# Performance work log

Hardware: AMD Instinct MI355X
Metric: run time of the kernel (lower is better)

## Reference

```python
import jax, jax.numpy as jnp
import numpy as np

# Config matching init_kwargs
DILATED = (1, 2, 3)
K = 4            # proto_size
P = 96           # num_prototypes
NUM_CLASSES = 2
E = 1024         # enc_size (bert-large)
EPS = 1e-8       # torch F.cosine_similarity eps
NUM_FILTERS = (32, 32, 32)  # P // len(DILATED) per dilation


def _neg_cosine_dist(batch, p_flat, d):
    """Replicates F.unfold(kernel=(K,1), dilation=d) + view(N,1,H,K*E) + -cosine_similarity.

    batch:  (N, S, E)
    p_flat: (n, K*E) -- protolayer slice flattened exactly as torch .view does
    returns (N, n, H) with H = S - d*(K-1)
    """
    N, S, _ = batch.shape
    H = S - d * (K - 1)
    # torch unfold output is (N, K, H*E) with element [n,k,h*E+e] = batch[n, h+k*d, e];
    # the subsequent .view(N,1,H,K*E) row-major reinterprets (K,H,E) -> (H, K*E).
    x = jnp.stack([batch[:, k * d:k * d + H, :] for k in range(K)], axis=1)  # (N, K, H, E)
    x = x.reshape(N, H, K * E)  # identical flattening to torch view
    dot = jnp.einsum('nhm,pm->nph', x, p_flat)              # (N, n, H)
    xn = jnp.maximum(jnp.linalg.norm(x, axis=-1), EPS)      # (N, H)
    pn = jnp.maximum(jnp.linalg.norm(p_flat, axis=-1), EPS)  # (n,)
    cos = dot / (xn[:, None, :] * pn[None, :, None])
    return -cos


def setup_inputs() -> dict:
    key = jax.random.key(0)
    k1, k2, k3 = jax.random.split(key, 3)
    N, S = 16, 512
    embedding = jax.random.normal(k1, (N, S, E), dtype=jnp.float32)
    mask = jnp.ones((N, S), dtype=jnp.int64)
    # nn.init.uniform_ default range [0, 1)
    protolayer = jax.random.uniform(k2, (P, E, K), dtype=jnp.float32)
    fc_w = jax.random.normal(k3, (NUM_CLASSES, P), dtype=jnp.float32) * 0.1
    return {"embedding": embedding, "mask": mask, "protolayer": protolayer, "fc_w": fc_w}


def reference(embedding, mask, protolayer, fc_w):
    # protolayer (P, E, K) -> (P, K*E) exactly as torch .view(1, P, 1, K*E)
    p_flat = protolayer.reshape(P, K * E)
    dists = []
    j = 0
    for d, n in zip(DILATED, NUM_FILTERS):
        dists.append(_neg_cosine_dist(embedding, p_flat[j:j + n], d))
        j += n
    # min-pool over sliding-window positions, concat over prototype groups
    prototype_distances = jnp.concatenate([jnp.min(x, axis=2) for x in dists], axis=1)  # (N, P)
    class_out = prototype_distances @ fc_w.T  # Linear(bias=False)
    return prototype_distances, class_out
```

## Files before the change

### kernel.cpp

```cpp
#include <hip/hip_runtime.h>
#include <stdint.h>

#define EE 1024
#define SS 512
#define NBATCH 16
#define PP 96
#define NROWS (NBATCH * SS)
#define NJ (PP * 4)
#define EPS 1e-8f

typedef __attribute__((ext_vector_type(8))) short bf16x8;
typedef __attribute__((ext_vector_type(4))) float f32x4;

__device__ __forceinline__ ushort f2bf(float f) {
    uint32_t u = __float_as_uint(f);
    u += 0x7fffu + ((u >> 16) & 1u);
    return (ushort)(u >> 16);
}

__device__ __forceinline__ void gload16(const void* g, void* l) {
    __builtin_amdgcn_global_load_lds(
        (const __attribute__((address_space(1))) uint32_t*)g,
        (__attribute__((address_space(3))) uint32_t*)l, 16, 0, 0);
}

__global__ __launch_bounds__(256) void conv_emb_kernel(const float* __restrict__ emb,
                                                       ushort* __restrict__ ebf,
                                                       float* __restrict__ rn2) {
    int r = blockIdx.x, t = threadIdx.x;
    float4 v = ((const float4*)(emb + (size_t)r * EE))[t];
    ((ushort4*)(ebf + (size_t)r * EE))[t] =
        make_ushort4(f2bf(v.x), f2bf(v.y), f2bf(v.z), f2bf(v.w));
    float s = v.x * v.x + v.y * v.y + v.z * v.z + v.w * v.w;
#pragma unroll
    for (int off = 32; off; off >>= 1) s += __shfl_down(s, off);
    __shared__ float red[4];
    if ((t & 63) == 0) red[t >> 6] = s;
    __syncthreads();
    if (t == 0) rn2[r] = red[0] + red[1] + red[2] + red[3];
}

__global__ __launch_bounds__(256) void conv_proto_kernel(const float* __restrict__ proto,
                                                         ushort* __restrict__ pbf,
                                                         float* __restrict__ pn) {
    int p = blockIdx.x, t = threadIdx.x;
    const float4* src = (const float4*)(proto + (size_t)p * 4096);
    ushort4* dst = (ushort4*)(pbf + (size_t)p * 4096);
    float s = 0.f;
#pragma unroll
    for (int i = 0; i < 4; i++) {
        float4 v = src[t + 256 * i];
        dst[t + 256 * i] = make_ushort4(f2bf(v.x), f2bf(v.y), f2bf(v.z), f2bf(v.w));
        s += v.x * v.x + v.y * v.y + v.z * v.z + v.w * v.w;
    }
#pragma unroll
    for (int off = 32; off; off >>= 1) s += __shfl_down(s, off);
    __shared__ float red[4];
    if ((t & 63) == 0) red[t >> 6] = s;
    __syncthreads();
    if (t == 0) pn[p] = sqrtf(red[0] + red[1] + red[2] + red[3]);
}

#define GBM 128
#define GBN 128
#define GBK 32

__global__ __launch_bounds__(256) void gemm_kernel(const ushort* __restrict__ A,
                                                   const ushort* __restrict__ B,
                                                   float* __restrict__ Rt,
                                                   int nsplit) {
    __shared__ ushort As[GBM * GBK];
    __shared__ ushort Bs[GBN * GBK];
    const int per = (NROWS / GBM) * (NJ / GBN);
    int bid = blockIdx.x;
    int split = bid / per;
    int rem = bid - split * per;
    int bm = rem & 63;
    int bn = rem >> 6;
    int klen = EE / nsplit;
    int kb = split * klen;
    int r0 = bm * GBM, j0 = bn * GBN;
    int tid = threadIdx.x;
    int lane = tid & 63;

    int srow = tid >> 2;
    int schunk = (tid & 3) ^ (srow & 3);
    const ushort* ga = A + (size_t)(r0 + srow) * EE + kb + schunk * 8;
    const ushort* gb = B + (size_t)(j0 + srow) * EE + kb + schunk * 8;
    ushort* lA = As + tid * 8;
    ushort* lB = Bs + tid * 8;

    int w = tid >> 6;
    int wm = (w >> 1) * 64, wn = (w & 1) * 64;
    int kc = lane >> 4;
    int fr = lane & 15;
    int fchunk = kc ^ (fr & 3);

    f32x4 acc[4][4] = {};

    for (int k0 = 0; k0 < klen; k0 += GBK) {
        __syncthreads();
        gload16(ga + k0, lA);
        gload16(ga + 64 * EE + k0, lA + 2048);
        gload16(gb + k0, lB);
        gload16(gb + 64 * EE + k0, lB + 2048);
        __syncthreads();
        bf16x8 af[4], bfr[4];
#pragma unroll
        for (int m = 0; m < 4; m++)
            af[m] = *(const bf16x8*)(As + (wm + m * 16 + fr) * GBK + fchunk * 8);
#pragma unroll
        for (int n = 0; n < 4; n++)
            bfr[n] = *(const bf16x8*)(Bs + (wn + n * 16 + fr) * GBK + fchunk * 8);
#pragma unroll
        for (int m = 0; m < 4; m++)
#pragma unroll
            for (int n = 0; n < 4; n++)
                acc[m][n] = __builtin_amdgcn_mfma_f32_16x16x32_bf16(af[m], bfr[n], acc[m][n], 0, 0, 0);
    }

    float* Rbase = Rt + (size_t)split * NJ * NROWS;
    int rloc = r0 + wm + (lane >> 4) * 4;
    int jloc = j0 + wn + fr;
#pragma unroll
    for (int m = 0; m < 4; m++)
#pragma unroll
        for (int n = 0; n < 4; n++)
            *(f32x4*)(Rbase + (size_t)(jloc + n * 16) * NROWS + rloc + m * 16) = acc[m][n];
}

__global__ __launch_bounds__(256) void combine_kernel(const float* __restrict__ Rt,
                                                      const float* __restrict__ rn2,
                                                      const float* __restrict__ pn,
                                                      float* __restrict__ out, int nsplit) {
    int wave = threadIdx.x >> 6;
    int lane = threadIdx.x & 63;
    int pair = blockIdx.x * 4 + wave;
    int n = pair / PP;
    int p = pair % PP;
    int d = (p >> 5) + 1;
    int H = SS - 3 * d;
    float pnv = fmaxf(pn[p], EPS);
    float best = -3.4e38f;
    for (int h = lane; h < H; h += 64) {
        float dot = 0.f, x2 = 0.f;
#pragma unroll
        for (int j = 0; j < 4; j++) {
            int q = h * 4 + j;
            int k = q / H;
            int s = q - k * H + k * d;
            int r = n * SS + s;
            size_t off = (size_t)(4 * p + j) * NROWS + r;
            float dv = Rt[off];
            if (nsplit == 2) dv += Rt[(size_t)NJ * NROWS + off];
            dot += dv;
            x2 += rn2[r];
        }
        float xn = fmaxf(sqrtf(x2), EPS);
        best = fmaxf(best, dot / (xn * pnv));
    }
#pragma unroll
    for (int off = 32; off; off >>= 1) best = fmaxf(best, __shfl_down(best, off));
    if (lane == 0) out[n * PP + p] = -best;
}

__global__ __launch_bounds__(64) void fc_kernel(const float* __restrict__ pd,
                                                const float* __restrict__ fcw,
                                                float* __restrict__ cls) {
    int t = threadIdx.x;
    if (t >= 32) return;
    int n = t >> 1, c = t & 1;
    float s = 0.f;
    for (int p = 0; p < PP; p++) s += pd[n * PP + p] * fcw[c * PP + p];
    cls[n * 2 + c] = s;
}

extern "C" void kernel_launch(void* const* d_in, const int* in_sizes, int n_in,
                              void* d_out, int out_size, void* d_ws, size_t ws_size,
                              hipStream_t stream) {
    const float* emb = (const float*)d_in[0];
    const float* proto = (const float*)d_in[2];
    const float* fcw = (const float*)d_in[3];
    float* out = (float*)d_out;

    uint8_t* ws = (uint8_t*)d_ws;
    ushort* ebf = (ushort*)ws;
    ushort* pbf = (ushort*)(ws + (size_t)NROWS * EE * 2);
    float* rn2 = (float*)(ws + (size_t)NROWS * EE * 2 + (size_t)NJ * EE * 2);
    float* pn = rn2 + NROWS;
    float* Rt = pn + 128;
    size_t fixed = (size_t)NROWS * EE * 2 + (size_t)NJ * EE * 2 + (size_t)(NROWS + 128) * 4;
    int nsplit = (ws_size >= fixed + 2 * (size_t)NJ * NROWS * 4) ? 2 : 1;

    conv_emb_kernel<<<NROWS, 256, 0, stream>>>(emb, ebf, rn2);
    conv_proto_kernel<<<PP, 256, 0, stream>>>(proto, pbf, pn);
    gemm_kernel<<<192 * nsplit, 256, 0, stream>>>(ebf, pbf, Rt, nsplit);
    combine_kernel<<<NBATCH * PP / 4, 256, 0, stream>>>(Rt, rn2, pn, out, nsplit);
    fc_kernel<<<1, 64, 0, stream>>>(out, fcw, out + NBATCH * PP);
}
```

Baseline: 53.66 us.

## Fuse conversion kernels, retile GEMM without split-K, fold FC into combine

Merges the embedding and prototype bf16 conversion into one launch, with one wave per embedding row. The GEMM is retiled to 64x128 tiles with a 64-wide K step and an 8-chunk swizzle, which replaces the split-K path with 384 blocks over the full K range. The final linear layer is folded into the combine kernel through atomicAdd onto a cls buffer zeroed with a memset. This reduces launch count and the extra split-K partial-sum traffic, but adds a memset launch and float atomics whose summation order is nondeterministic.

```diff
diff --git a/kernel.cpp b/kernel.cpp
--- a/kernel.cpp
+++ b/kernel.cpp
@@ -24,115 +24,129 @@
         (__attribute__((address_space(3))) uint32_t*)l, 16, 0, 0);
 }
 
-__global__ __launch_bounds__(256) void conv_emb_kernel(const float* __restrict__ emb,
-                                                       ushort* __restrict__ ebf,
-                                                       float* __restrict__ rn2) {
-    int r = blockIdx.x, t = threadIdx.x;
-    float4 v = ((const float4*)(emb + (size_t)r * EE))[t];
-    ((ushort4*)(ebf + (size_t)r * EE))[t] =
-        make_ushort4(f2bf(v.x), f2bf(v.y), f2bf(v.z), f2bf(v.w));
-    float s = v.x * v.x + v.y * v.y + v.z * v.z + v.w * v.w;
-#pragma unroll
-    for (int off = 32; off; off >>= 1) s += __shfl_down(s, off);
-    __shared__ float red[4];
-    if ((t & 63) == 0) red[t >> 6] = s;
-    __syncthreads();
-    if (t == 0) rn2[r] = red[0] + red[1] + red[2] + red[3];
-}
-
-__global__ __launch_bounds__(256) void conv_proto_kernel(const float* __restrict__ proto,
-                                                         ushort* __restrict__ pbf,
-                                                         float* __restrict__ pn) {
-    int p = blockIdx.x, t = threadIdx.x;
-    const float4* src = (const float4*)(proto + (size_t)p * 4096);
-    ushort4* dst = (ushort4*)(pbf + (size_t)p * 4096);
-    float s = 0.f;
-#pragma unroll
-    for (int i = 0; i < 4; i++) {
-        float4 v = src[t + 256 * i];
-        dst[t + 256 * i] = make_ushort4(f2bf(v.x), f2bf(v.y), f2bf(v.z), f2bf(v.w));
-        s += v.x * v.x + v.y * v.y + v.z * v.z + v.w * v.w;
-    }
-#pragma unroll
-    for (int off = 32; off; off >>= 1) s += __shfl_down(s, off);
-    __shared__ float red[4];
-    if ((t & 63) == 0) red[t >> 6] = s;
-    __syncthreads();
-    if (t == 0) pn[p] = sqrtf(red[0] + red[1] + red[2] + red[3]);
-}
-
-#define GBM 128
+__global__ __launch_bounds__(256) void conv_kernel(const float* __restrict__ emb,
+                                                   const float* __restrict__ proto,
+                                                   ushort* __restrict__ ebf,
+                                                   ushort* __restrict__ pbf,
+                                                   float* __restrict__ rn2,
+                                                   float* __restrict__ pn) {
+    int b = blockIdx.x, t = threadIdx.x;
+    if (b < NROWS / 4) {
+        int r = b * 4 + (t >> 6);
+        int l = t & 63;
+        const float4* src = (const float4*)(emb + (size_t)r * EE);
+        ushort4* dst = (ushort4*)(ebf + (size_t)r * EE);
+        float s = 0.f;
+#pragma unroll
+        for (int i = 0; i < 4; i++) {
+            float4 v = src[l + 64 * i];
+            dst[l + 64 * i] = make_ushort4(f2bf(v.x), f2bf(v.y), f2bf(v.z), f2bf(v.w));
+            s += v.x * v.x + v.y * v.y + v.z * v.z + v.w * v.w;
+        }
+#pragma unroll
+        for (int off = 32; off; off >>= 1) s += __shfl_down(s, off);
+        if (l == 0) rn2[r] = s;
+    } else {
+        int p = b - NROWS / 4;
+        const float4* src = (const float4*)(proto + (size_t)p * 4096);
+        ushort4* dst = (ushort4*)(pbf + (size_t)p * 4096);
+        float s = 0.f;
+#pragma unroll
+        for (int i = 0; i < 4; i++) {
+            float4 v = src[t + 256 * i];
+            dst[t + 256 * i] = make_ushort4(f2bf(v.x), f2bf(v.y), f2bf(v.z), f2bf(v.w));
+            s += v.x * v.x + v.y * v.y + v.z * v.z + v.w * v.w;
+        }
+#pragma unroll
+        for (int off = 32; off; off >>= 1) s += __shfl_down(s, off);
+        __shared__ float red[4];
+        if ((t & 63) == 0) red[t >> 6] = s;
+        __syncthreads();
+        if (t == 0) pn[p] = sqrtf(red[0] + red[1] + red[2] + red[3]);
+    }
+}
+
+#define GBM 64
 #define GBN 128
-#define GBK 32
+#define GBK 64
 
 __global__ __launch_bounds__(256) void gemm_kernel(const ushort* __restrict__ A,
                                                    const ushort* __restrict__ B,
-                                                   float* __restrict__ Rt,
-                                                   int nsplit) {
+                                                   float* __restrict__ Rt) {
     __shared__ ushort As[GBM * GBK];
     __shared__ ushort Bs[GBN * GBK];
-    const int per = (NROWS / GBM) * (NJ / GBN);
-    int bid = blockIdx.x;
-    int split = bid / per;
-    int rem = bid - split * per;
-    int bm = rem & 63;
-    int bn = rem >> 6;
-    int klen = EE / nsplit;
-    int kb = split * klen;
+    int bn = blockIdx.x >> 7;
+    int bm = blockIdx.x & 127;
     int r0 = bm * GBM, j0 = bn * GBN;
     int tid = threadIdx.x;
     int lane = tid & 63;
 
-    int srow = tid >> 2;
-    int schunk = (tid & 3) ^ (srow & 3);
-    const ushort* ga = A + (size_t)(r0 + srow) * EE + kb + schunk * 8;
-    const ushort* gb = B + (size_t)(j0 + srow) * EE + kb + schunk * 8;
+    int srow = tid >> 3;
+    int gc = (tid & 7) ^ (srow & 7);
+    const ushort* ga = A + (size_t)(r0 + srow) * EE + gc * 8;
+    const ushort* gb = B + (size_t)(j0 + srow) * EE + gc * 8;
     ushort* lA = As + tid * 8;
     ushort* lB = Bs + tid * 8;
 
     int w = tid >> 6;
-    int wm = (w >> 1) * 64, wn = (w & 1) * 64;
+    int wm = (w >> 1) * 32, wn = (w & 1) * 64;
     int kc = lane >> 4;
     int fr = lane & 15;
-    int fchunk = kc ^ (fr & 3);
-
-    f32x4 acc[4][4] = {};
-
-    for (int k0 = 0; k0 < klen; k0 += GBK) {
+
+    f32x4 acc[2][4] = {};
+
+    for (int k0 = 0; k0 < EE; k0 += GBK) {
         __syncthreads();
         gload16(ga + k0, lA);
-        gload16(ga + 64 * EE + k0, lA + 2048);
+        gload16(ga + 32 * EE + k0, lA + 2048);
         gload16(gb + k0, lB);
-        gload16(gb + 64 * EE + k0, lB + 2048);
+        gload16(gb + 32 * EE + k0, lB + 2048);
+        gload16(gb + 64 * EE + k0, lB + 4096);
+        gload16(gb + 96 * EE + k0, lB + 6144);
         __syncthreads();
-        bf16x8 af[4], bfr[4];
-#pragma unroll
-        for (int m = 0; m < 4; m++)
-            af[m] = *(const bf16x8*)(As + (wm + m * 16 + fr) * GBK + fchunk * 8);
-#pragma unroll
-        for (int n = 0; n < 4; n++)
-            bfr[n] = *(const bf16x8*)(Bs + (wn + n * 16 + fr) * GBK + fchunk * 8);
-#pragma unroll
-        for (int m = 0; m < 4; m++)
+        bf16x8 af[2][2], bf[4][2];
+#pragma unroll
+        for (int m = 0; m < 2; m++) {
+            int row = wm + m * 16 + fr;
+#pragma unroll
+            for (int kk = 0; kk < 2; kk++) {
+                int cc = (kk * 4 + kc) ^ (row & 7);
+                af[m][kk] = *(const bf16x8*)(As + row * GBK + cc * 8);
+            }
+        }
+#pragma unroll
+        for (int n = 0; n < 4; n++) {
+            int row = wn + n * 16 + fr;
+#pragma unroll
+            for (int kk = 0; kk < 2; kk++) {
+                int cc = (kk * 4 + kc) ^ (row & 7);
+                bf[n][kk] = *(const bf16x8*)(Bs + row * GBK + cc * 8);
+            }
+        }
+#pragma unroll
+        for (int m = 0; m < 2; m++)
 #pragma unroll
             for (int n = 0; n < 4; n++)
-                acc[m][n] = __builtin_amdgcn_mfma_f32_16x16x32_bf16(af[m], bfr[n], acc[m][n], 0, 0, 0);
-    }
-
-    float* Rbase = Rt + (size_t)split * NJ * NROWS;
+#pragma unroll
+                for (int kk = 0; kk < 2; kk++)
+                    acc[m][n] = __builtin_amdgcn_mfma_f32_16x16x32_bf16(af[m][kk], bf[n][kk], acc[m][n], 0, 0, 0);
+    }
+
     int rloc = r0 + wm + (lane >> 4) * 4;
     int jloc = j0 + wn + fr;
 #pragma unroll
-    for (int m = 0; m < 4; m++)
+    for (int m = 0; m < 2; m++)
 #pragma unroll
         for (int n = 0; n < 4; n++)
-            *(f32x4*)(Rbase + (size_t)(jloc + n * 16) * NROWS + rloc + m * 16) = acc[m][n];
+            *(f32x4*)(Rt + (size_t)(jloc + n * 16) * NROWS + rloc + m * 16) = acc[m][n];
 }
 
 __global__ __launch_bounds__(256) void combine_kernel(const float* __restrict__ Rt,
                                                       const float* __restrict__ rn2,
                                                       const float* __restrict__ pn,
-                                                      float* __restrict__ out, int nsplit) {
+                                                      const float* __restrict__ fcw,
+                                                      float* __restrict__ out,
+                                                      float* __restrict__ cls) {
     int wave = threadIdx.x >> 6;
     int lane = threadIdx.x & 63;
     int pair = blockIdx.x * 4 + wave;
@@ -150,10 +164,7 @@
             int k = q / H;
             int s = q - k * H + k * d;
             int r = n * SS + s;
-            size_t off = (size_t)(4 * p + j) * NROWS + r;
-            float dv = Rt[off];
-            if (nsplit == 2) dv += Rt[(size_t)NJ * NROWS + off];
-            dot += dv;
+            dot += Rt[(size_t)(4 * p + j) * NROWS + r];
             x2 += rn2[r];
         }
         float xn = fmaxf(sqrtf(x2), EPS);
@@ -161,18 +172,12 @@
     }
 #pragma unroll
     for (int off = 32; off; off >>= 1) best = fmaxf(best, __shfl_down(best, off));
-    if (lane == 0) out[n * PP + p] = -best;
-}
-
-__global__ __launch_bounds__(64) void fc_kernel(const float* __restrict__ pd,
-                                                const float* __restrict__ fcw,
-                                                float* __restrict__ cls) {
-    int t = threadIdx.x;
-    if (t >= 32) return;
-    int n = t >> 1, c = t & 1;
-    float s = 0.f;
-    for (int p = 0; p < PP; p++) s += pd[n * PP + p] * fcw[c * PP + p];
-    cls[n * 2 + c] = s;
+    if (lane == 0) {
+        float pdv = -best;
+        out[n * PP + p] = pdv;
+        atomicAdd(&cls[n * 2 + 0], pdv * fcw[p]);
+        atomicAdd(&cls[n * 2 + 1], pdv * fcw[PP + p]);
+    }
 }
 
 extern "C" void kernel_launch(void* const* d_in, const int* in_sizes, int n_in,
@@ -182,6 +187,7 @@
     const float* proto = (const float*)d_in[2];
     const float* fcw = (const float*)d_in[3];
     float* out = (float*)d_out;
+    float* cls = out + NBATCH * PP;
 
     uint8_t* ws = (uint8_t*)d_ws;
     ushort* ebf = (ushort*)ws;
@@ -189,12 +195,9 @@
     float* rn2 = (float*)(ws + (size_t)NROWS * EE * 2 + (size_t)NJ * EE * 2);
     float* pn = rn2 + NROWS;
     float* Rt = pn + 128;
-    size_t fixed = (size_t)NROWS * EE * 2 + (size_t)NJ * EE * 2 + (size_t)(NROWS + 128) * 4;
-    int nsplit = (ws_size >= fixed + 2 * (size_t)NJ * NROWS * 4) ? 2 : 1;
-
-    conv_emb_kernel<<<NROWS, 256, 0, stream>>>(emb, ebf, rn2);
-    conv_proto_kernel<<<PP, 256, 0, stream>>>(proto, pbf, pn);
-    gemm_kernel<<<192 * nsplit, 256, 0, stream>>>(ebf, pbf, Rt, nsplit);
-    combine_kernel<<<NBATCH * PP / 4, 256, 0, stream>>>(Rt, rn2, pn, out, nsplit);
-    fc_kernel<<<1, 64, 0, stream>>>(out, fcw, out + NBATCH * PP);
-}
+
+    hipMemsetAsync(cls, 0, NBATCH * 2 * sizeof(float), stream);
+    conv_kernel<<<NROWS / 4 + PP, 256, 0, stream>>>(emb, proto, ebf, pbf, rn2, pn);
+    gemm_kernel<<<3 * 128, 256, 0, stream>>>(ebf, pbf, Rt);
+    combine_kernel<<<NBATCH * PP / 4, 256, 0, stream>>>(Rt, rn2, pn, fcw, out, cls);
+}
```

Result: slower. 61.93 us (+15.4%).
